# Performance work log

Hardware: AMD Instinct MI355X
Metric: run time of the kernel (lower is better)

The kernel has to match this reference:

```python
import jax, jax.numpy as jnp
import numpy as np

HIDDEN = 1024
HEADS = 16
HEAD_DIM = HIDDEN // HEADS
MAX_SEQ = 2048
BATCH = 2
SEQ = 2048


def setup_inputs() -> dict:
    key = jax.random.key(0)
    ks = jax.random.split(key, 6)
    x = jax.random.normal(ks[0], (BATCH, SEQ, HIDDEN), dtype=jnp.float32)
    # torch Linear params expressed as [in, out] weight + bias
    W1 = jax.random.normal(ks[1], (HIDDEN, 4 * HIDDEN), dtype=jnp.float32) * (HIDDEN ** -0.5)
    b1 = jnp.zeros((4 * HIDDEN,), dtype=jnp.float32)
    W2 = jax.random.normal(ks[2], (HIDDEN, HIDDEN), dtype=jnp.float32) * (HIDDEN ** -0.5)
    b2 = jnp.zeros((HIDDEN,), dtype=jnp.float32)
    rel_table = jax.random.normal(ks[3], (2 * MAX_SEQ - 1, HEADS), dtype=jnp.float32) * 0.02
    # causal mask [B, S, S]; True = keep
    attn_mask = jnp.broadcast_to(jnp.tril(jnp.ones((SEQ, SEQ), dtype=bool)), (BATCH, SEQ, SEQ))
    return {"x": x, "W1": W1, "b1": b1, "W2": W2, "b2": b2,
            "rel_table": rel_table, "attn_mask": attn_mask}


def reference(x, W1, b1, W2, b2, rel_table, attn_mask):
    B, S, H = x.shape
    # fused projection + SiLU, then chunk into U, Q, K, V
    activated = jax.nn.silu(jnp.einsum('bsh,hf->bsf', x, W1) + b1)
    U, Qp, Kp, Vp = jnp.split(activated, 4, axis=-1)
    # [B, nH, S, hd]
    def heads(t):
        return t.reshape(B, S, HEADS, HEAD_DIM).transpose(0, 2, 1, 3)
    Q, K, V = heads(Qp), heads(Kp), heads(Vp)
    scale = HEAD_DIM ** -0.5
    scores = jnp.einsum('bnqd,bnkd->bnqk', Q, K) * scale
    # relative position bias gather: idx[i,j] = i - j + MAX_SEQ - 1
    pos = jnp.arange(S)
    rel_idx = pos[:, None] - pos[None, :] + (MAX_SEQ - 1)  # [S, S]
    rel_bias = rel_table[rel_idx].transpose(2, 0, 1)[None]  # [1, nH, S, S]
    scores = scores + rel_bias
    attn = jax.nn.silu(scores)
    attn = jnp.where(attn_mask[:, None, :, :], attn, 0.0)
    out = jnp.einsum('bnqk,bnkd->bnqd', attn, V)
    out = out.transpose(0, 2, 1, 3).reshape(B, S, H)
    gated = out * U
    return jnp.einsum('bsh,hf->bsf', gated, W2) + b2
```

## Files before the change

kernel.cpp:

```cpp
#include <hip/hip_runtime.h>
#include <hip/hip_bf16.h>
#include <math.h>

#define HIDDEN   1024
#define HEADS    16
#define HEAD_DIM 64
#define SEQ      2048
#define BATCH    2
#define FDIM     4096
#define MTOT     4096
#define MAXSEQ   2048

typedef __bf16 bf16x8 __attribute__((ext_vector_type(8)));
typedef float  f32x4  __attribute__((ext_vector_type(4)));
typedef unsigned short u16;

__device__ __forceinline__ float silu_fast(float v) {
    return v * __builtin_amdgcn_rcpf(1.f + __expf(-v));
}

__device__ __forceinline__ u16 f2bf(float f) {
    union { float f; unsigned u; } v; v.f = f;
    unsigned r = v.u + 0x7FFFu + ((v.u >> 16) & 1u);
    return (u16)(r >> 16);
}
__device__ __forceinline__ float bf2f(u16 b) {
    union { unsigned u; float f; } v; v.u = ((unsigned)b) << 16;
    return v.f;
}
__device__ __forceinline__ unsigned pk2(float a, float b) {
    union { __hip_bfloat162 h; unsigned u; } z;
    z.h = __float22bfloat162_rn(make_float2(a, b));
    return z.u;
}

__device__ __forceinline__ void gload16(const void* g, void* l) {
    __builtin_amdgcn_global_load_lds(
        (const __attribute__((address_space(1))) void*)g,
        (__attribute__((address_space(3))) void*)l, 16, 0, 0);
}

__global__ __launch_bounds__(256) void prep_kernel(
    const float* __restrict__ X, const float* __restrict__ W1,
    const float* __restrict__ W2,
    u16* __restrict__ Xb, u16* __restrict__ W1t, u16* __restrict__ W2t,
    unsigned* __restrict__ ticket)
{
    __shared__ u16 T[64][72];
    const int tid = threadIdx.x;
    const int bid = blockIdx.x;

    if (bid == 0 && tid == 0) *ticket = 0u;

    if (bid < 2048) {
        int idx = (bid * 256 + tid) * 8;
        float4 a = *(const float4*)&X[idx];
        float4 b = *(const float4*)&X[idx + 4];
        uint4 pk = make_uint4(pk2(a.x, a.y), pk2(a.z, a.w),
                              pk2(b.x, b.y), pk2(b.z, b.w));
        *(uint4*)&Xb[idx] = pk;
        return;
    }

    const float* W; u16* Wt; int rows, cols, r0, c0;
    if (bid < 3072) {
        int t = bid - 2048;
        W = W1; Wt = W1t; rows = HIDDEN; cols = FDIM;
        c0 = (t & 63) * 64; r0 = (t >> 6) * 64;
    } else {
        int t = bid - 3072;
        W = W2; Wt = W2t; rows = HIDDEN; cols = HIDDEN;
        c0 = (t & 15) * 64; r0 = (t >> 4) * 64;
    }
#pragma unroll
    for (int l = 0; l < 4; ++l) {
        int idx = tid + l * 256;
        int row = idx >> 4;
        int c4  = (idx & 15) * 4;
        float4 v = *(const float4*)&W[(size_t)(r0 + row) * cols + c0 + c4];
        T[c4 + 0][row] = f2bf(v.x);
        T[c4 + 1][row] = f2bf(v.y);
        T[c4 + 2][row] = f2bf(v.z);
        T[c4 + 3][row] = f2bf(v.w);
    }
    __syncthreads();
#pragma unroll
    for (int l = 0; l < 2; ++l) {
        int idx = tid + l * 256;
        int row = idx >> 3;
        int cb  = (idx & 7) * 8;
        *(float4*)&Wt[(size_t)(c0 + row) * rows + r0 + cb] = *(float4*)&T[row][cb];
    }
}

#define GEMM_CORE(A_PTR, BT_PTR, KDIM, BM_, BN_, WMW, WNW)                     \
    enum { MTI = (BM_) / (WMW) / 16, NTI = (BN_) / (WNW) / 16,                 \
           ACH = (BM_) / 8, BCH = (BN_) / 8 };                                 \
    __shared__ __align__(16) u16 As[(BM_) * 64];                               \
    __shared__ __align__(16) u16 Bs[(BN_) * 64];                               \
    const int tid  = threadIdx.x;                                              \
    const int lane = tid & 63;                                                 \
    const int w    = tid >> 6;                                                 \
    const int wm   = w % (WMW), wn = w / (WMW);                                \
    const int l16  = lane & 15, quad = lane >> 4;                              \
    const int m0   = blockIdx.y * (BM_);                                       \
    const int n0   = blockIdx.x * (BN_);                                       \
    const int srow = lane >> 3;                                                \
    const int scol = (((lane & 7) ^ srow)) * 8;     \
    const int xr   = l16 & 7;                           \
    f32x4 acc[MTI][NTI];                                                       \
    _Pragma("unroll")                                                          \
    for (int mt = 0; mt < MTI; ++mt)                                           \
        _Pragma("unroll")                                                      \
        for (int nt = 0; nt < NTI; ++nt)                                       \
            acc[mt][nt] = (f32x4){0.f, 0.f, 0.f, 0.f};                         \
    for (int k0 = 0; k0 < (KDIM); k0 += 64) {                                  \
        __syncthreads();                                                       \
        _Pragma("unroll")                                                      \
        for (int ci = w; ci < ACH; ci += 4) {                                  \
            unsigned off = __builtin_amdgcn_readfirstlane(ci * 1024);          \
            gload16(&(A_PTR)[(size_t)(m0 + ci * 8 + srow) * (KDIM) + k0 + scol],\
                    (char*)As + off);                                          \
        }                                                                      \
        _Pragma("unroll")                                                      \
        for (int ci = w; ci < BCH; ci += 4) {                                  \
            unsigned off = __builtin_amdgcn_readfirstlane(ci * 1024);          \
            gload16(&(BT_PTR)[(size_t)(n0 + ci * 8 + srow) * (KDIM) + k0 + scol],\
                    (char*)Bs + off);                                          \
        }                                                                      \
        __syncthreads();                                                       \
        _Pragma("unroll")                                                      \
        for (int kc = 0; kc < 2; ++kc) {                                       \
            bf16x8 af[MTI], bfr[NTI];                                          \
            const int gsw = ((kc * 4 + quad) ^ xr) * 8;                        \
            _Pragma("unroll")                                                  \
            for (int t = 0; t < MTI; ++t)                                      \
                af[t]  = *(const bf16x8*)&As[(wm * (BM_ / WMW) + t * 16 + l16) \
                                             * 64 + gsw];                      \
            _Pragma("unroll")                                                  \
            for (int t = 0; t < NTI; ++t)                                      \
                bfr[t] = *(const bf16x8*)&Bs[(wn * (BN_ / WNW) + t * 16 + l16) \
                                             * 64 + gsw];                      \
            _Pragma("unroll")                                                  \
            for (int mt = 0; mt < MTI; ++mt)                                   \
                _Pragma("unroll")                                              \
                for (int nt = 0; nt < NTI; ++nt)                               \
                    acc[mt][nt] = __builtin_amdgcn_mfma_f32_16x16x32_bf16(     \
                        bfr[nt], af[mt], acc[mt][nt], 0, 0, 0);                \
        }                                                                      \
    }

__global__ __launch_bounds__(256) void gemm1_mfma_kernel(
    const u16* __restrict__ A, const u16* __restrict__ Bt,
    const float* __restrict__ b1,
    u16* __restrict__ Ub, u16* __restrict__ Qh,
    u16* __restrict__ Kh, u16* __restrict__ Vh)
{
    GEMM_CORE(A, Bt, HIDDEN, 128, 128, 2, 2)

    const int chunk = n0 >> 10;
    u16* dstbase = (chunk == 0) ? Ub : (chunk == 1) ? Qh : (chunk == 2) ? Kh : Vh;
    const float postscale = (chunk == 1) ? 0.125f : 1.0f;

    float4 bias4[NTI]; int nloc[NTI];
#pragma unroll
    for (int nt = 0; nt < NTI; ++nt) {
        int nb = n0 + wn * 64 + nt * 16 + quad * 4;
        bias4[nt] = *(const float4*)&b1[nb];
        nloc[nt] = nb & 1023;
    }
#pragma unroll
    for (int mt = 0; mt < MTI; ++mt) {
        int m  = m0 + wm * 64 + mt * 16 + l16;
        int bb = m >> 11, s = m & 2047;
#pragma unroll
        for (int nt = 0; nt < NTI; ++nt) {
            float v0 = silu_fast(acc[mt][nt][0] + bias4[nt].x) * postscale;
            float v1 = silu_fast(acc[mt][nt][1] + bias4[nt].y) * postscale;
            float v2 = silu_fast(acc[mt][nt][2] + bias4[nt].z) * postscale;
            float v3 = silu_fast(acc[mt][nt][3] + bias4[nt].w) * postscale;
            uint2 pk = make_uint2(pk2(v0, v1), pk2(v2, v3));
            size_t o;
            if (chunk == 0) {
                o = (size_t)m * 1024 + nloc[nt];
            } else {
                int h = nloc[nt] >> 6, d = nloc[nt] & 63;
                o = (size_t)(((bb * HEADS + h) * SEQ) + s) * HEAD_DIM + d;
            }
            *(uint2*)&dstbase[o] = pk;
        }
    }
}

__global__ __launch_bounds__(256) void gemm2_mfma_kernel(
    const u16* __restrict__ A, const u16* __restrict__ Bt,
    const float* __restrict__ b2, float* __restrict__ Out)
{
    GEMM_CORE(A, Bt, HIDDEN, 64, 128, 1, 4)

    float4 bias4[NTI]; int nb[NTI];
#pragma unroll
    for (int nt = 0; nt < NTI; ++nt) {
        nb[nt] = n0 + wn * 32 + nt * 16 + quad * 4;
        bias4[nt] = *(const float4*)&b2[nb[nt]];
    }
#pragma unroll
    for (int mt = 0; mt < MTI; ++mt) {
        int m = m0 + mt * 16 + l16;
#pragma unroll
        for (int nt = 0; nt < NTI; ++nt) {
            float4 vv;
            vv.x = acc[mt][nt][0] + bias4[nt].x;
            vv.y = acc[mt][nt][1] + bias4[nt].y;
            vv.z = acc[mt][nt][2] + bias4[nt].z;
            vv.w = acc[mt][nt][3] + bias4[nt].w;
            *(float4*)&Out[(size_t)m * 1024 + nb[nt]] = vv;
        }
    }
}

__global__ __launch_bounds__(256, 3) void attn_mfma_kernel(
    const u16* __restrict__ Qh, const u16* __restrict__ Kh,
    const u16* __restrict__ Vh, const float* __restrict__ rel,
    const u16* __restrict__ Ub, u16* __restrict__ G,
    unsigned* __restrict__ ticket)
{
    __shared__ __align__(16) u16 Ks[128][72];
    __shared__ __align__(16) u16 Vt[64][136];
    __shared__ float rel_sh[192];
    __shared__ unsigned sh_t;

    const int tid  = threadIdx.x;
    const int lane = tid & 63;
    const int w    = tid >> 6;
    const int quad = lane >> 4;
    const int l16  = lane & 15;
    const int ws   = w & 1;
    const int pp   = w >> 1;
    const int qbase = ws * 32;

    const int k_r = tid >> 3,       k_c = (tid & 7) * 8;
    const int v_k = (tid & 31) * 2, v_d = (tid >> 5) * 8;

    for (;;) {
        if (tid == 0) sh_t = atomicAdd(ticket, 1u);
        __syncthreads();
        const unsigned t = sh_t;
        if (t >= 1024u) return;

        const int qt = 31 - (int)(t >> 5);
        const int bh = (int)(t & 31u);
        const int h  = bh & 15;
        const int bb = bh >> 4;
        const int q0 = qt * 64;

        const u16* Kg = Kh + (size_t)((bb * HEADS + h) * SEQ) * HEAD_DIM;
        const u16* Vg = Vh + (size_t)((bb * HEADS + h) * SEQ) * HEAD_DIM;
        const u16* Qg = Qh + (size_t)((bb * HEADS + h) * SEQ + q0) * HEAD_DIM;

        bf16x8 qa[2][2];
#pragma unroll
        for (int sub = 0; sub < 2; ++sub) {
            const int qr = qbase + sub * 16 + l16;
            qa[sub][0] = *(const bf16x8*)&Qg[qr * HEAD_DIM + quad * 8];
            qa[sub][1] = *(const bf16x8*)&Qg[qr * HEAD_DIM + 32 + quad * 8];
        }

        float4 kA0 = *(const float4*)&Kg[(size_t)k_r * 64 + k_c];
        float4 kA1 = *(const float4*)&Kg[(size_t)(k_r + 32) * 64 + k_c];
        float4 vA0 = *(const float4*)&Vg[(size_t)v_k * 64 + v_d];
        float4 vA1 = *(const float4*)&Vg[(size_t)(v_k + 1) * 64 + v_d];
        float4 kB0, kB1, vB0, vB1;
        if (qt >= 1) {
            kB0 = *(const float4*)&Kg[(size_t)(64 + k_r) * 64 + k_c];
            kB1 = *(const float4*)&Kg[(size_t)(64 + k_r + 32) * 64 + k_c];
            vB0 = *(const float4*)&Vg[(size_t)(64 + v_k) * 64 + v_d];
            vB1 = *(const float4*)&Vg[(size_t)(64 + v_k + 1) * 64 + v_d];
        }
        float relreg = 0.f;
        if (tid < 191) relreg = rel[(size_t)(q0 + 1920 + tid) * HEADS + h];

        f32x4 o[2][4];
#pragma unroll
        for (int sub = 0; sub < 2; ++sub)
#pragma unroll
            for (int dt = 0; dt < 4; ++dt) o[sub][dt] = (f32x4){0.f, 0.f, 0.f, 0.f};

        for (int ip = 0; 2 * ip <= qt; ++ip) {
            const int kp = ip * 128;
            const bool hasB = (2 * ip + 1 <= qt);

            *(float4*)&Ks[k_r][k_c]      = kA0;
            *(float4*)&Ks[k_r + 32][k_c] = kA1;
            {
                union { float4 f; u16 u[8]; } a0, a1;
                a0.f = vA0; a1.f = vA1;
#pragma unroll
                for (int i = 0; i < 8; ++i)
                    *(unsigned*)&Vt[v_d + i][v_k] =
                        (unsigned)a0.u[i] | ((unsigned)a1.u[i] << 16);
            }
            if (hasB) {
                *(float4*)&Ks[64 + k_r][k_c]      = kB0;
                *(float4*)&Ks[64 + k_r + 32][k_c] = kB1;
                union { float4 f; u16 u[8]; } a0, a1;
                a0.f = vB0; a1.f = vB1;
#pragma unroll
                for (int i = 0; i < 8; ++i)
                    *(unsigned*)&Vt[v_d + i][64 + v_k] =
                        (unsigned)a0.u[i] | ((unsigned)a1.u[i] << 16);
            }
            if (tid < 191) rel_sh[tid] = relreg;
            __syncthreads();

            {
                const int nk0 = 2 * ip + 2;
                if (nk0 <= qt) {
                    const int b0 = nk0 * 64;
                    kA0 = *(const float4*)&Kg[(size_t)(b0 + k_r) * 64 + k_c];
                    kA1 = *(const float4*)&Kg[(size_t)(b0 + k_r + 32) * 64 + k_c];
                    vA0 = *(const float4*)&Vg[(size_t)(b0 + v_k) * 64 + v_d];
                    vA1 = *(const float4*)&Vg[(size_t)(b0 + v_k + 1) * 64 + v_d];
                    if (tid < 191)
                        relreg = rel[(size_t)(q0 - kp - 128 + 1920 + tid) * HEADS + h];
                    if (nk0 + 1 <= qt) {
                        const int b1 = b0 + 64;
                        kB0 = *(const float4*)&Kg[(size_t)(b1 + k_r) * 64 + k_c];
                        kB1 = *(const float4*)&Kg[(size_t)(b1 + k_r + 32) * 64 + k_c];
                        vB0 = *(const float4*)&Vg[(size_t)(b1 + v_k) * 64 + v_d];
                        vB1 = *(const float4*)&Vg[(size_t)(b1 + v_k + 1) * 64 + v_d];
                    }
                }
            }

            const int myc = 2 * ip + pp;
            if (myc <= qt) {
                const int ko      = pp * 64;
                const int relofs  = pp ? 63 : 127;
                const bool diag   = (myc == qt);
                const int qrelb   = q0 - kp - ko;

                union bfu { unsigned u[4]; bf16x8 v; };
                bfu pa0[2], pa1[2];

#pragma unroll
                for (int cp = 0; cp < 2; ++cp) {
                    unsigned dw[2][2][2];
#pragma unroll
                    for (int cl = 0; cl < 2; ++cl) {
                        const int ct = cp * 2 + cl;
                        bf16x8 ka0 = *(const bf16x8*)&Ks[ko + ct * 16 + l16][quad * 8];
                        bf16x8 ka1 = *(const bf16x8*)&Ks[ko + ct * 16 + l16][32 + quad * 8];
#pragma unroll
                        for (int sub = 0; sub < 2; ++sub) {
                            f32x4 sc = {0.f, 0.f, 0.f, 0.f};
                            sc = __builtin_amdgcn_mfma_f32_16x16x32_bf16(ka0, qa[sub][0], sc, 0, 0, 0);
                            sc = __builtin_amdgcn_mfma_f32_16x16x32_bf16(ka1, qa[sub][1], sc, 0, 0, 0);
                            const int qrow = qbase + sub * 16 + l16;
                            const int ib   = qrow - ct * 16 - quad * 4 + relofs;
                            float p4[4];
                            if (diag) {
#pragma unroll
                                for (int r = 0; r < 4; ++r) {
                                    float s = sc[r] + rel_sh[ib - r];
                                    int kloc = ct * 16 + quad * 4 + r;
                                    p4[r] = (qrelb + qrow - kloc >= 0) ? silu_fast(s) : 0.f;
                                }
                            } else {
#pragma unroll
                                for (int r = 0; r < 4; ++r) {
                                    float s = sc[r] + rel_sh[ib - r];
                                    p4[r] = silu_fast(s);
                                }
                            }
                            dw[sub][cl][0] = pk2(p4[0], p4[1]);
                            dw[sub][cl][1] = pk2(p4[2], p4[3]);
                        }
                    }
                    bfu* pa = cp ? pa1 : pa0;
#pragma unroll
                    for (int sub = 0; sub < 2; ++sub) {
#pragma unroll
                        for (int s = 0; s < 2; ++s) {
                            auto a = __builtin_amdgcn_permlane32_swap(
                                dw[sub][0][s], dw[sub][1][s], false, false);
                            auto x = __builtin_amdgcn_permlane16_swap(
                                a[0], a[1], false, false);
                            pa[sub].u[s]     = x[0];
                            pa[sub].u[2 + s] = x[1];
                        }
                    }
                }

#pragma unroll
                for (int dt = 0; dt < 4; ++dt) {
                    bf16x8 vb0 = *(const bf16x8*)&Vt[dt * 16 + l16][ko + quad * 8];
                    bf16x8 vb1 = *(const bf16x8*)&Vt[dt * 16 + l16][ko + 32 + quad * 8];
#pragma unroll
                    for (int sub = 0; sub < 2; ++sub) {
                        o[sub][dt] = __builtin_amdgcn_mfma_f32_16x16x32_bf16(pa0[sub].v, vb0, o[sub][dt], 0, 0, 0);
                        o[sub][dt] = __builtin_amdgcn_mfma_f32_16x16x32_bf16(pa1[sub].v, vb1, o[sub][dt], 0, 0, 0);
                    }
                }
            }
            __syncthreads();
        }

        float* Ored = (float*)&Ks[0][0];
        if (pp == 1) {
#pragma unroll
            for (int sub = 0; sub < 2; ++sub)
#pragma unroll
                for (int dt = 0; dt < 4; ++dt)
                    *(f32x4*)&Ored[((ws << 3) + (sub << 2) + dt) * 256 + lane * 4] =
                        o[sub][dt];
        }
        __syncthreads();
        if (pp == 0) {
#pragma unroll
            for (int sub = 0; sub < 2; ++sub)
#pragma unroll
                for (int dt = 0; dt < 4; ++dt) {
                    f32x4 r4 = *(const f32x4*)&Ored[((ws << 3) + (sub << 2) + dt) * 256 + lane * 4];
                    o[sub][dt] += r4;
#pragma unroll
                    for (int r = 0; r < 4; ++r) {
                        int q = q0 + qbase + sub * 16 + quad * 4 + r;
                        size_t base = (size_t)(bb * SEQ + q) * HIDDEN +
                                      h * HEAD_DIM + dt * 16 + l16;
                        float u = bf2f(Ub[base]);
                        G[base] = f2bf(o[sub][dt][r] * u);
                    }
                }
        }
    }
}

extern "C" void kernel_launch(void* const* d_in, const int* in_sizes, int n_in,
                              void* d_out, int out_size, void* d_ws, size_t ws_size,
                              hipStream_t stream)
{
    const float* X   = (const float*)d_in[0];
    const float* W1  = (const float*)d_in[1];
    const float* b1  = (const float*)d_in[2];
    const float* W2  = (const float*)d_in[3];
    const float* b2  = (const float*)d_in[4];
    const float* rel = (const float*)d_in[5];
    float* out = (float*)d_out;

    const size_t MH = (size_t)MTOT * HIDDEN;
    u16* Ub   = (u16*)d_ws;
    u16* Qh   = Ub  + MH;
    u16* Kh   = Qh  + MH;
    u16* Vh   = Kh  + MH;
    u16* Gbuf = Vh  + MH;
    u16* Xb   = Gbuf + MH;
    u16* W1t  = Xb  + MH;
    u16* W2t  = W1t + MH;
    unsigned* ticket = (unsigned*)(W2t + (size_t)HIDDEN * HIDDEN);

    prep_kernel<<<3328, 256, 0, stream>>>(X, W1, W2, Xb, W1t, W2t, ticket);
    gemm1_mfma_kernel<<<dim3(FDIM / 128, MTOT / 128), 256, 0, stream>>>(
        Xb, W1t, b1, Ub, Qh, Kh, Vh);
    attn_mfma_kernel<<<dim3(1024), 256, 0, stream>>>(
        Qh, Kh, Vh, rel, Ub, Gbuf, ticket);
    gemm2_mfma_kernel<<<dim3(HIDDEN / 128, MTOT / 64), 256, 0, stream>>>(
        Gbuf, W2t, b2, out);
}
```

Baseline: 230.0 us.

## Use 128-row query tiles per block and drop split-K partial reduction

The attention kernel now processes 128 query rows per work item, with each of the four waves owning 32 rows. Previously it handled 64 rows with two waves splitting the key chunks, which then needed a reduction of partial outputs through shared memory. Each staged K/V tile now serves twice as many queries, and the cross-wave reduction and its extra barrier are gone. The persistent grid shrinks to 384 blocks over 512 tickets. The trade-off is fewer, larger work items, which risks worse load balance across CUs for the causal triangle, and waves on the diagonal tile skip whole chunks and sit idle.

```diff
diff --git a/kernel.cpp b/kernel.cpp
--- a/kernel.cpp
+++ b/kernel.cpp
@@ -227,7 +227,7 @@
 {
     __shared__ __align__(16) u16 Ks[128][72];
     __shared__ __align__(16) u16 Vt[64][136];
-    __shared__ float rel_sh[192];
+    __shared__ float rel_sh[256];
     __shared__ unsigned sh_t;
 
     const int tid  = threadIdx.x;
@@ -235,9 +235,7 @@
     const int w    = tid >> 6;
     const int quad = lane >> 4;
     const int l16  = lane & 15;
-    const int ws   = w & 1;
-    const int pp   = w >> 1;
-    const int qbase = ws * 32;
+    const int qbase = w * 32;
 
     const int k_r = tid >> 3,       k_c = (tid & 7) * 8;
     const int v_k = (tid & 31) * 2, v_d = (tid >> 5) * 8;
@@ -246,13 +244,13 @@
         if (tid == 0) sh_t = atomicAdd(ticket, 1u);
         __syncthreads();
         const unsigned t = sh_t;
-        if (t >= 1024u) return;
-
-        const int qt = 31 - (int)(t >> 5);
+        if (t >= 512u) return;
+
+        const int qt = 15 - (int)(t >> 5);
         const int bh = (int)(t & 31u);
         const int h  = bh & 15;
         const int bb = bh >> 4;
-        const int q0 = qt * 64;
+        const int q0 = qt * 128;
 
         const u16* Kg = Kh + (size_t)((bb * HEADS + h) * SEQ) * HEAD_DIM;
         const u16* Vg = Vh + (size_t)((bb * HEADS + h) * SEQ) * HEAD_DIM;
@@ -268,17 +266,14 @@
 
         float4 kA0 = *(const float4*)&Kg[(size_t)k_r * 64 + k_c];
         float4 kA1 = *(const float4*)&Kg[(size_t)(k_r + 32) * 64 + k_c];
+        float4 kB0 = *(const float4*)&Kg[(size_t)(64 + k_r) * 64 + k_c];
+        float4 kB1 = *(const float4*)&Kg[(size_t)(64 + k_r + 32) * 64 + k_c];
         float4 vA0 = *(const float4*)&Vg[(size_t)v_k * 64 + v_d];
         float4 vA1 = *(const float4*)&Vg[(size_t)(v_k + 1) * 64 + v_d];
-        float4 kB0, kB1, vB0, vB1;
-        if (qt >= 1) {
-            kB0 = *(const float4*)&Kg[(size_t)(64 + k_r) * 64 + k_c];
-            kB1 = *(const float4*)&Kg[(size_t)(64 + k_r + 32) * 64 + k_c];
-            vB0 = *(const float4*)&Vg[(size_t)(64 + v_k) * 64 + v_d];
-            vB1 = *(const float4*)&Vg[(size_t)(64 + v_k + 1) * 64 + v_d];
-        }
+        float4 vB0 = *(const float4*)&Vg[(size_t)(64 + v_k) * 64 + v_d];
+        float4 vB1 = *(const float4*)&Vg[(size_t)(64 + v_k + 1) * 64 + v_d];
         float relreg = 0.f;
-        if (tid < 191) relreg = rel[(size_t)(q0 + 1920 + tid) * HEADS + h];
+        if (tid < 255) relreg = rel[(size_t)(q0 + 1920 + tid) * HEADS + h];
 
         f32x4 o[2][4];
 #pragma unroll
@@ -286,59 +281,48 @@
 #pragma unroll
             for (int dt = 0; dt < 4; ++dt) o[sub][dt] = (f32x4){0.f, 0.f, 0.f, 0.f};
 
-        for (int ip = 0; 2 * ip <= qt; ++ip) {
+        for (int ip = 0; ip <= qt; ++ip) {
             const int kp = ip * 128;
-            const bool hasB = (2 * ip + 1 <= qt);
-
-            *(float4*)&Ks[k_r][k_c]      = kA0;
-            *(float4*)&Ks[k_r + 32][k_c] = kA1;
+
+            *(float4*)&Ks[k_r][k_c]           = kA0;
+            *(float4*)&Ks[k_r + 32][k_c]      = kA1;
+            *(float4*)&Ks[64 + k_r][k_c]      = kB0;
+            *(float4*)&Ks[64 + k_r + 32][k_c] = kB1;
             {
-                union { float4 f; u16 u[8]; } a0, a1;
-                a0.f = vA0; a1.f = vA1;
-#pragma unroll
-                for (int i = 0; i < 8; ++i)
+                union { float4 f; u16 u[8]; } a0, a1, b0u, b1u;
+                a0.f = vA0; a1.f = vA1; b0u.f = vB0; b1u.f = vB1;
+#pragma unroll
+                for (int i = 0; i < 8; ++i) {
                     *(unsigned*)&Vt[v_d + i][v_k] =
                         (unsigned)a0.u[i] | ((unsigned)a1.u[i] << 16);
-            }
-            if (hasB) {
-                *(float4*)&Ks[64 + k_r][k_c]      = kB0;
-                *(float4*)&Ks[64 + k_r + 32][k_c] = kB1;
-                union { float4 f; u16 u[8]; } a0, a1;
-                a0.f = vB0; a1.f = vB1;
-#pragma unroll
-                for (int i = 0; i < 8; ++i)
                     *(unsigned*)&Vt[v_d + i][64 + v_k] =
-                        (unsigned)a0.u[i] | ((unsigned)a1.u[i] << 16);
-            }
-            if (tid < 191) rel_sh[tid] = relreg;
-            __syncthreads();
-
-            {
-                const int nk0 = 2 * ip + 2;
-                if (nk0 <= qt) {
-                    const int b0 = nk0 * 64;
-                    kA0 = *(const float4*)&Kg[(size_t)(b0 + k_r) * 64 + k_c];
-                    kA1 = *(const float4*)&Kg[(size_t)(b0 + k_r + 32) * 64 + k_c];
-                    vA0 = *(const float4*)&Vg[(size_t)(b0 + v_k) * 64 + v_d];
-                    vA1 = *(const float4*)&Vg[(size_t)(b0 + v_k + 1) * 64 + v_d];
-                    if (tid < 191)
-                        relreg = rel[(size_t)(q0 - kp - 128 + 1920 + tid) * HEADS + h];
-                    if (nk0 + 1 <= qt) {
-                        const int b1 = b0 + 64;
-                        kB0 = *(const float4*)&Kg[(size_t)(b1 + k_r) * 64 + k_c];
-                        kB1 = *(const float4*)&Kg[(size_t)(b1 + k_r + 32) * 64 + k_c];
-                        vB0 = *(const float4*)&Vg[(size_t)(b1 + v_k) * 64 + v_d];
-                        vB1 = *(const float4*)&Vg[(size_t)(b1 + v_k + 1) * 64 + v_d];
-                    }
+                        (unsigned)b0u.u[i] | ((unsigned)b1u.u[i] << 16);
                 }
             }
-
-            const int myc = 2 * ip + pp;
-            if (myc <= qt) {
-                const int ko      = pp * 64;
-                const int relofs  = pp ? 63 : 127;
-                const bool diag   = (myc == qt);
-                const int qrelb   = q0 - kp - ko;
+            if (tid < 255) rel_sh[tid] = relreg;
+            __syncthreads();
+
+            if (ip < qt) {
+                const int b0 = (2 * ip + 2) * 64;
+                const int b1 = b0 + 64;
+                kA0 = *(const float4*)&Kg[(size_t)(b0 + k_r) * 64 + k_c];
+                kA1 = *(const float4*)&Kg[(size_t)(b0 + k_r + 32) * 64 + k_c];
+                kB0 = *(const float4*)&Kg[(size_t)(b1 + k_r) * 64 + k_c];
+                kB1 = *(const float4*)&Kg[(size_t)(b1 + k_r + 32) * 64 + k_c];
+                vA0 = *(const float4*)&Vg[(size_t)(b0 + v_k) * 64 + v_d];
+                vA1 = *(const float4*)&Vg[(size_t)(b0 + v_k + 1) * 64 + v_d];
+                vB0 = *(const float4*)&Vg[(size_t)(b1 + v_k) * 64 + v_d];
+                vB1 = *(const float4*)&Vg[(size_t)(b1 + v_k + 1) * 64 + v_d];
+                if (tid < 255)
+                    relreg = rel[(size_t)(q0 - kp - 128 + 1920 + tid) * HEADS + h];
+            }
+
+            const bool diag = (ip == qt);
+
+#pragma unroll
+            for (int pc = 0; pc < 2; ++pc) {
+                const int ko = pc * 64;
+                if (diag && qbase + 31 < ko) continue;
 
                 union bfu { unsigned u[4]; bf16x8 v; };
                 bfu pa0[2], pa1[2];
@@ -357,14 +341,14 @@
                             sc = __builtin_amdgcn_mfma_f32_16x16x32_bf16(ka0, qa[sub][0], sc, 0, 0, 0);
                             sc = __builtin_amdgcn_mfma_f32_16x16x32_bf16(ka1, qa[sub][1], sc, 0, 0, 0);
                             const int qrow = qbase + sub * 16 + l16;
-                            const int ib   = qrow - ct * 16 - quad * 4 + relofs;
+                            const int ib   = qrow - ct * 16 - quad * 4 + 127 - ko;
                             float p4[4];
                             if (diag) {
 #pragma unroll
                                 for (int r = 0; r < 4; ++r) {
                                     float s = sc[r] + rel_sh[ib - r];
                                     int kloc = ct * 16 + quad * 4 + r;
-                                    p4[r] = (qrelb + qrow - kloc >= 0) ? silu_fast(s) : 0.f;
+                                    p4[r] = (qrow - ko - kloc >= 0) ? silu_fast(s) : 0.f;
                                 }
                             } else {
 #pragma unroll
@@ -406,33 +390,18 @@
             __syncthreads();
         }
 
-        float* Ored = (float*)&Ks[0][0];
-        if (pp == 1) {
-#pragma unroll
-            for (int sub = 0; sub < 2; ++sub)
-#pragma unroll
-                for (int dt = 0; dt < 4; ++dt)
-                    *(f32x4*)&Ored[((ws << 3) + (sub << 2) + dt) * 256 + lane * 4] =
-                        o[sub][dt];
-        }
-        __syncthreads();
-        if (pp == 0) {
-#pragma unroll
-            for (int sub = 0; sub < 2; ++sub)
-#pragma unroll
-                for (int dt = 0; dt < 4; ++dt) {
-                    f32x4 r4 = *(const f32x4*)&Ored[((ws << 3) + (sub << 2) + dt) * 256 + lane * 4];
-                    o[sub][dt] += r4;
-#pragma unroll
-                    for (int r = 0; r < 4; ++r) {
-                        int q = q0 + qbase + sub * 16 + quad * 4 + r;
-                        size_t base = (size_t)(bb * SEQ + q) * HIDDEN +
-                                      h * HEAD_DIM + dt * 16 + l16;
-                        float u = bf2f(Ub[base]);
-                        G[base] = f2bf(o[sub][dt][r] * u);
-                    }
+#pragma unroll
+        for (int sub = 0; sub < 2; ++sub)
+#pragma unroll
+            for (int dt = 0; dt < 4; ++dt)
+#pragma unroll
+                for (int r = 0; r < 4; ++r) {
+                    int q = q0 + qbase + sub * 16 + quad * 4 + r;
+                    size_t base = (size_t)(bb * SEQ + q) * HIDDEN +
+                                  h * HEAD_DIM + dt * 16 + l16;
+                    float u = bf2f(Ub[base]);
+                    G[base] = f2bf(o[sub][dt][r] * u);
                 }
-        }
     }
 }
 
@@ -462,7 +431,7 @@
     prep_kernel<<<3328, 256, 0, stream>>>(X, W1, W2, Xb, W1t, W2t, ticket);
     gemm1_mfma_kernel<<<dim3(FDIM / 128, MTOT / 128), 256, 0, stream>>>(
         Xb, W1t, b1, Ub, Qh, Kh, Vh);
-    attn_mfma_kernel<<<dim3(1024), 256, 0, stream>>>(
+    attn_mfma_kernel<<<dim3(384), 256, 0, stream>>>(
         Qh, Kh, Vh, rel, Ub, Gbuf, ticket);
     gemm2_mfma_kernel<<<dim3(HIDDEN / 128, MTOT / 64), 256, 0, stream>>>(
         Gbuf, W2t, b2, out);
```

After: 231.8 us. No clear change (+0.8%).
